# Kernel tuning notes

Measured on AMD Instinct MI355X. Metric: run time of the kernel, lower is better.

The kernel has to match this reference:

```python
import jax, jax.numpy as jnp
import numpy as np

N_NODES = 100000
N_EDGES = 800000
D_IN = 100
D_HID = 100
N_CLS = 16


def setup_inputs() -> dict:
    key = jax.random.key(0)
    ks = jax.random.split(key, 7)
    x = jax.random.normal(ks[0], (N_NODES, D_IN), dtype=jnp.float32)
    edge_index = jax.random.randint(ks[1], (2, N_EDGES), 0, N_NODES, dtype=jnp.int64)
    s = 1.0 / np.sqrt(D_IN)
    Wl = jax.random.normal(ks[2], (D_HID, D_IN), dtype=jnp.float32) * s
    bl = jax.random.normal(ks[3], (D_HID,), dtype=jnp.float32) * s
    Wr = jax.random.normal(ks[4], (D_HID, D_IN), dtype=jnp.float32) * s
    sc = 1.0 / np.sqrt(D_HID)
    Wc = jax.random.normal(ks[5], (N_CLS, D_HID), dtype=jnp.float32) * sc
    bc = jax.random.normal(ks[6], (N_CLS,), dtype=jnp.float32) * sc
    return {"x": x, "edge_index": edge_index, "Wl": Wl, "bl": bl,
            "Wr": Wr, "Wc": Wc, "bc": bc}


def reference(x, edge_index, Wl, bl, Wr, Wc, bc):
    # SAGEConv (mean aggregation): out_i = Wl @ mean_{j in N(i)} x_j + bl + Wr @ x_i
    src, dst = edge_index[0], edge_index[1]
    n = x.shape[0]
    agg = jax.ops.segment_sum(x[src], dst, num_segments=n)          # [N, D_IN]
    deg = jax.ops.segment_sum(jnp.ones((src.shape[0],), x.dtype), dst, num_segments=n)
    mean = agg / jnp.maximum(deg, 1.0)[:, None]
    h = mean @ Wl.T + bl + x @ Wr.T                                  # [N, D_HID]
    h = jax.nn.relu(h)
    out = h @ Wc.T + bc                                              # [N, N_CLS]
    return out
```

## Files before the change

### kernel.cpp

```cpp
#include <hip/hip_runtime.h>
#include <hip/hip_bf16.h>
#include <hip/hip_fp16.h>

#define N_NODES 100000
#define N_EDGES 800000
#define D_IN 100
#define D_HID 100
#define N_CLS 16

#define TN 64
#define SK 232
#define AK 200
#define SCHUNK 1024
#define SNBLK 98

typedef _Float16 f16x8 __attribute__((ext_vector_type(8)));
typedef _Float16 f16x4 __attribute__((ext_vector_type(4)));
typedef float f32x4 __attribute__((ext_vector_type(4)));

#define RANK_SLOT(e) (((e) >> 7) * AK + ((e) & 127))

__global__ __launch_bounds__(256) void hist_k(const int* __restrict__ ei,
                                              int* __restrict__ cnt,
                                              unsigned short* __restrict__ rank16)
{
    const int e = blockIdx.x * 256 + threadIdx.x;
    if (e < N_EDGES) {
        const int dst = ei[N_EDGES + e];
        const int r = atomicAdd(&cnt[dst], 1);
        rank16[RANK_SLOT(e)] = (unsigned short)r;
    }
}

__global__ __launch_bounds__(256) void scan_a(const int* __restrict__ cnt,
                                              int* __restrict__ bsum)
{
    __shared__ int red[256];
    const int t = threadIdx.x;
    const int base = blockIdx.x * SCHUNK + t * 4;
    int s = 0;
    if (base + 3 < N_NODES) {
        const int4 v = *reinterpret_cast<const int4*>(cnt + base);
        s = v.x + v.y + v.z + v.w;
    } else {
        for (int i = 0; i < 4; ++i)
            if (base + i < N_NODES) s += cnt[base + i];
    }
    red[t] = s;
    __syncthreads();
    for (int d = 128; d > 0; d >>= 1) {
        if (t < d) red[t] += red[t + d];
        __syncthreads();
    }
    if (t == 0) bsum[blockIdx.x] = red[0];
}

__global__ __launch_bounds__(256) void scan_c(const int* __restrict__ cnt,
                                              const int* __restrict__ bsum,
                                              int* __restrict__ wofs)
{
    __shared__ int red[256];
    __shared__ int sb[128];
    const int t = threadIdx.x;
    if (t < 128) sb[t] = (t < SNBLK) ? bsum[t] : 0;
    __syncthreads();
    for (int d = 1; d < 128; d <<= 1) {
        int a = 0;
        if (t < 128) { a = sb[t]; if (t >= d) a += sb[t - d]; }
        __syncthreads();
        if (t < 128) sb[t] = a;
        __syncthreads();
    }
    const int bofs = sb[blockIdx.x] - bsum[blockIdx.x];
    if (blockIdx.x == 0 && t == 0) wofs[N_NODES] = sb[SNBLK - 1];

    const int base = blockIdx.x * SCHUNK + t * 4;
    int c0 = 0, c1 = 0, c2 = 0, c3 = 0;
    if (base + 3 < N_NODES) {
        const int4 v = *reinterpret_cast<const int4*>(cnt + base);
        c0 = v.x; c1 = v.y; c2 = v.z; c3 = v.w;
    } else {
        if (base + 0 < N_NODES) c0 = cnt[base + 0];
        if (base + 1 < N_NODES) c1 = cnt[base + 1];
        if (base + 2 < N_NODES) c2 = cnt[base + 2];
        if (base + 3 < N_NODES) c3 = cnt[base + 3];
    }
    const int s = c0 + c1 + c2 + c3;
    red[t] = s;
    __syncthreads();
    for (int d = 1; d < 256; d <<= 1) {
        const int a = red[t];
        const int add = (t >= d) ? red[t - d] : 0;
        __syncthreads();
        red[t] = a + add;
        __syncthreads();
    }
    int prefix = bofs + red[t] - s;
    const int c[4] = {c0, c1, c2, c3};
    for (int i = 0; i < 4; ++i) {
        const int idx = base + i;
        if (idx < N_NODES) {
            wofs[idx] = prefix;
            prefix += c[i];
        }
    }
}

__global__ __launch_bounds__(256) void fill_csr(const int* __restrict__ ei,
                                                const int* __restrict__ wofs,
                                                const unsigned short* __restrict__ rank16,
                                                int* __restrict__ esrc)
{
    const int e = blockIdx.x * 256 + threadIdx.x;
    if (e >= N_EDGES) return;
    const int src = ei[e];
    const int dst = ei[N_EDGES + e];
    const int pos = wofs[dst] + (int)rank16[RANK_SLOT(e)];
    esrc[pos] = src;
}

__global__ __launch_bounds__(256) void cvt_w16(const float* __restrict__ Wl,
                                               const float* __restrict__ Wr,
                                               _Float16* __restrict__ w16)
{
    const int idx = blockIdx.x * 256 + threadIdx.x;
    if (idx >= 128 * 58) return;
    const int o = idx / 58, s = idx - o * 58;
    const int k0 = s * 4;
    float4 v = make_float4(0.f, 0.f, 0.f, 0.f);
    if (o < 100) {
        if (s < 25)       v = *reinterpret_cast<const float4*>(Wl + o * 100 + k0);
        else if (s < 50)  v = *reinterpret_cast<const float4*>(Wr + o * 100 + (k0 - 100));
    }
    f16x4 h = { (_Float16)v.x, (_Float16)v.y, (_Float16)v.z, (_Float16)v.w };
    *reinterpret_cast<f16x4*>(w16 + o * SK + k0) = h;
}

__global__ __launch_bounds__(256) void cvt_x16(const float* __restrict__ x,
                                               _Float16* __restrict__ amx)
{
    const int idx = blockIdx.x * 256 + threadIdx.x;
    if (idx >= N_NODES * 25) return;
    const int n = idx / 25, s = idx - n * 25;
    const float4 v = *reinterpret_cast<const float4*>(x + (long)n * D_IN + s * 4);
    f16x4 h = { (_Float16)v.x, (_Float16)v.y, (_Float16)v.z, (_Float16)v.w };
    *reinterpret_cast<f16x4*>(amx + (long)n * AK + 100 + s * 4) = h;
}

__global__ __launch_bounds__(256) void gather_mean(
    const int* __restrict__ wofs, const int* __restrict__ esrc,
    _Float16* __restrict__ amx)
{
    const int node = blockIdx.x * 8 + (threadIdx.x >> 5);
    if (node >= N_NODES) return;
    const int l = threadIdx.x & 31;
    const int r0 = wofs[node];
    const int r1 = wofs[node + 1];
    const int deg = r1 - r0;

    float4 acc = make_float4(0.f, 0.f, 0.f, 0.f);
    for (int base = 0; base < deg; base += 32) {
        int s = 0;
        if (base + l < deg) s = esrc[r0 + base + l];
        const int rem = deg - base;
        const int m = rem < 32 ? rem : 32;
        for (int j = 0; j < m; ++j) {
            const int src = __shfl(s, j, 32);
            if (l < 25) {
                const f16x4 v = *reinterpret_cast<const f16x4*>(
                    amx + (long)src * AK + 100 + l * 4);
                acc.x += (float)v[0]; acc.y += (float)v[1];
                acc.z += (float)v[2]; acc.w += (float)v[3];
            }
        }
    }
    if (l < 25) {
        const float inv = 1.0f / fmaxf((float)deg, 1.0f);
        f16x4 h = { (_Float16)(acc.x * inv), (_Float16)(acc.y * inv),
                    (_Float16)(acc.z * inv), (_Float16)(acc.w * inv) };
        *reinterpret_cast<f16x4*>(amx + (long)node * AK + l * 4) = h;
    }
}

__global__ __launch_bounds__(512, 1) void sage_node(
    const _Float16* __restrict__ amx, const _Float16* __restrict__ w16,
    const float* __restrict__ bl, const float* __restrict__ Wc,
    const float* __restrict__ bc, float* __restrict__ out)
{
    __shared__ __align__(16) _Float16 wS[128 * SK];
    __shared__ __align__(16) _Float16 aS[TN * SK];
    __shared__ float wcS[16 * 100];
    __shared__ float blS[128];
    __shared__ float bcS[16];

    const int tid = threadIdx.x;
    const int wid = tid >> 6;
    const int lane = tid & 63;
    const int node0 = blockIdx.x * TN;

    for (int c = tid; c < 128 * 29; c += 512) {
        const f16x8 v = *reinterpret_cast<const f16x8*>(w16 + c * 8);
        *reinterpret_cast<f16x8*>(wS + c * 8) = v;
    }
    {
        const f16x8 z = { (_Float16)0.f, (_Float16)0.f, (_Float16)0.f, (_Float16)0.f,
                          (_Float16)0.f, (_Float16)0.f, (_Float16)0.f, (_Float16)0.f };
        const _Float16* ga = amx + (size_t)node0 * AK;
        for (int c = tid; c < 64 * 29; c += 512) {
            const int row = c / 29, j = c - row * 29;
            f16x8 v = z;
            if (j < 25) v = *reinterpret_cast<const f16x8*>(ga + row * AK + j * 8);
            *reinterpret_cast<f16x8*>(aS + row * SK + j * 8) = v;
        }
    }
    for (int i = tid; i < 1600; i += 512) wcS[i] = Wc[i];
    if (tid < 128) blS[tid] = (tid < 100) ? bl[tid] : 0.0f;
    if (tid < 16)  bcS[tid] = bc[tid];
    __syncthreads();

    const int wr = wid >> 2;
    const int wq = wid & 3;
    const int lrow = lane & 15;
    const int lk = (lane >> 4) * 8;

    f32x4 acc00 = {0.f, 0.f, 0.f, 0.f}, acc01 = acc00, acc10 = acc00, acc11 = acc00;
    const _Float16* aB = aS + (wr * 32 + lrow) * SK + lk;
    const _Float16* bB = wS + (wq * 32 + lrow) * SK + lk;

    #pragma unroll
    for (int ks = 0; ks < 7; ++ks) {
        const f16x8 a0 = *reinterpret_cast<const f16x8*>(aB + ks * 32);
        const f16x8 a1 = *reinterpret_cast<const f16x8*>(aB + 16 * SK + ks * 32);
        const f16x8 b0 = *reinterpret_cast<const f16x8*>(bB + ks * 32);
        const f16x8 b1 = *reinterpret_cast<const f16x8*>(bB + 16 * SK + ks * 32);
        acc00 = __builtin_amdgcn_mfma_f32_16x16x32_f16(a0, b0, acc00, 0, 0, 0);
        acc01 = __builtin_amdgcn_mfma_f32_16x16x32_f16(a0, b1, acc01, 0, 0, 0);
        acc10 = __builtin_amdgcn_mfma_f32_16x16x32_f16(a1, b0, acc10, 0, 0, 0);
        acc11 = __builtin_amdgcn_mfma_f32_16x16x32_f16(a1, b1, acc11, 0, 0, 0);
    }
    __syncthreads();

    float* hS = reinterpret_cast<float*>(wS);
    const int crow = (lane >> 4) * 4;
    const int ccol = lane & 15;
    #pragma unroll
    for (int mi = 0; mi < 2; ++mi) {
        #pragma unroll
        for (int ni = 0; ni < 2; ++ni) {
            const f32x4 a = (mi == 0) ? (ni == 0 ? acc00 : acc01)
                                      : (ni == 0 ? acc10 : acc11);
            const int o = wq * 32 + ni * 16 + ccol;
            #pragma unroll
            for (int r = 0; r < 4; ++r) {
                const int nl = wr * 32 + mi * 16 + crow + r;
                if (o < 104)
                    hS[nl * 104 + o] = fmaxf(a[r] + blS[o], 0.0f);
            }
        }
    }
    __syncthreads();

    {
        const int nl = tid >> 3;
        const int q = tid & 7;
        float o0 = bcS[2 * q], o1 = bcS[2 * q + 1];
        const float* hP = hS + nl * 104;
        const float* w0 = wcS + (2 * q) * 100;
        const float* w1 = wcS + (2 * q + 1) * 100;
        for (int o = 0; o < 100; o += 4) {
            const float4 h4 = *reinterpret_cast<const float4*>(hP + o);
            const float4 a = *reinterpret_cast<const float4*>(w0 + o);
            const float4 b = *reinterpret_cast<const float4*>(w1 + o);
            o0 += h4.x * a.x + h4.y * a.y + h4.z * a.z + h4.w * a.w;
            o1 += h4.x * b.x + h4.y * b.y + h4.z * b.z + h4.w * b.w;
        }
        const int node = node0 + nl;
        if (node < N_NODES)
            *reinterpret_cast<float2*>(out + (long)node * N_CLS + 2 * q) =
                make_float2(o0, o1);
    }
}

extern "C" void kernel_launch(void* const* d_in, const int* in_sizes, int n_in,
                              void* d_out, int out_size, void* d_ws, size_t ws_size,
                              hipStream_t stream) {
    const float* x  = (const float*)d_in[0];
    const int*   ei = (const int*)d_in[1];
    const float* Wl = (const float*)d_in[2];
    const float* bl = (const float*)d_in[3];
    const float* Wr = (const float*)d_in[4];
    const float* Wc = (const float*)d_in[5];
    const float* bc = (const float*)d_in[6];
    float* out = (float*)d_out;

    int* cnt    = (int*)d_ws;
    int* wofs   = cnt + N_NODES;
    int* esrc   = wofs + N_NODES + 4;
    int* bsum   = esrc + N_EDGES;
    _Float16* w16 = (_Float16*)(bsum + 128);
    _Float16* amx = w16 + 128 * SK;
    unsigned short* rank16 = (unsigned short*)amx;

    hipMemsetAsync(cnt, 0, N_NODES * sizeof(int), stream);

    hist_k<<<(N_EDGES + 255) / 256, 256, 0, stream>>>(ei, cnt, rank16);
    scan_a<<<SNBLK, 256, 0, stream>>>(cnt, bsum);
    scan_c<<<SNBLK, 256, 0, stream>>>(cnt, bsum, wofs);
    fill_csr<<<(N_EDGES + 255) / 256, 256, 0, stream>>>(ei, wofs, rank16, esrc);
    cvt_w16<<<(128 * 58 + 255) / 256, 256, 0, stream>>>(Wl, Wr, w16);
    cvt_x16<<<(N_NODES * 25 + 255) / 256, 256, 0, stream>>>(x, amx);
    gather_mean<<<(N_NODES + 7) / 8, 256, 0, stream>>>(wofs, esrc, amx);

    sage_node<<<(N_NODES + TN - 1) / TN, 512, 0, stream>>>(
        amx, w16, bl, Wc, bc, out);
}
```

Measured before the change: 240.8 us.

## Merge prep kernels, double node tile, and use MFMA for classifier layer

Fuses the weight conversion into the scan-A kernel and the x conversion into the CSR fill kernel, cutting two launches and letting independent work run concurrently. The rank scratch slot mapping changes so it occupies only the mean columns of amx, avoiding a clash with the x columns that are now written in the same launch. The node kernel tile grows to 128 nodes so each wave does more MFMAs per weight load, and the hidden activations are stored as fp16 so the 16-class output layer runs on MFMA instead of scalar FMAs. This adds fp16 rounding of hidden activations and classifier weights, and uses more LDS per block.

```diff
diff --git a/kernel.cpp b/kernel.cpp
--- a/kernel.cpp
+++ b/kernel.cpp
@@ -8,17 +8,19 @@
 #define D_HID 100
 #define N_CLS 16
 
-#define TN 64
+#define TN 128
 #define SK 232
 #define AK 200
+#define HSTR 136
 #define SCHUNK 1024
 #define SNBLK 98
+#define FBLK 3125
 
 typedef _Float16 f16x8 __attribute__((ext_vector_type(8)));
 typedef _Float16 f16x4 __attribute__((ext_vector_type(4)));
 typedef float f32x4 __attribute__((ext_vector_type(4)));
 
-#define RANK_SLOT(e) (((e) >> 7) * AK + ((e) & 127))
+#define RANK_SLOT(e) (((e) / 100) * AK + ((e) % 100))
 
 __global__ __launch_bounds__(256) void hist_k(const int* __restrict__ ei,
                                               int* __restrict__ cnt,
@@ -32,27 +34,43 @@
     }
 }
 
-__global__ __launch_bounds__(256) void scan_a(const int* __restrict__ cnt,
-                                              int* __restrict__ bsum)
-{
-    __shared__ int red[256];
+__global__ __launch_bounds__(256) void scanA_cvtW(
+    const int* __restrict__ cnt, int* __restrict__ bsum,
+    const float* __restrict__ Wl, const float* __restrict__ Wr,
+    _Float16* __restrict__ w16)
+{
     const int t = threadIdx.x;
-    const int base = blockIdx.x * SCHUNK + t * 4;
-    int s = 0;
-    if (base + 3 < N_NODES) {
-        const int4 v = *reinterpret_cast<const int4*>(cnt + base);
-        s = v.x + v.y + v.z + v.w;
+    if (blockIdx.x < SNBLK) {
+        __shared__ int red[256];
+        const int base = blockIdx.x * SCHUNK + t * 4;
+        int s = 0;
+        if (base + 3 < N_NODES) {
+            const int4 v = *reinterpret_cast<const int4*>(cnt + base);
+            s = v.x + v.y + v.z + v.w;
+        } else {
+            for (int i = 0; i < 4; ++i)
+                if (base + i < N_NODES) s += cnt[base + i];
+        }
+        red[t] = s;
+        __syncthreads();
+        for (int d = 128; d > 0; d >>= 1) {
+            if (t < d) red[t] += red[t + d];
+            __syncthreads();
+        }
+        if (t == 0) bsum[blockIdx.x] = red[0];
     } else {
-        for (int i = 0; i < 4; ++i)
-            if (base + i < N_NODES) s += cnt[base + i];
-    }
-    red[t] = s;
-    __syncthreads();
-    for (int d = 128; d > 0; d >>= 1) {
-        if (t < d) red[t] += red[t + d];
-        __syncthreads();
-    }
-    if (t == 0) bsum[blockIdx.x] = red[0];
+        const int idx = (blockIdx.x - SNBLK) * 256 + t;
+        if (idx >= 128 * 58) return;
+        const int o = idx / 58, s = idx - o * 58;
+        const int k0 = s * 4;
+        float4 v = make_float4(0.f, 0.f, 0.f, 0.f);
+        if (o < 100) {
+            if (s < 25)       v = *reinterpret_cast<const float4*>(Wl + o * 100 + k0);
+            else if (s < 50)  v = *reinterpret_cast<const float4*>(Wr + o * 100 + (k0 - 100));
+        }
+        f16x4 h = { (_Float16)v.x, (_Float16)v.y, (_Float16)v.z, (_Float16)v.w };
+        *reinterpret_cast<f16x4*>(w16 + o * SK + k0) = h;
+    }
 }
 
 __global__ __launch_bounds__(256) void scan_c(const int* __restrict__ cnt,
@@ -106,45 +124,27 @@
     }
 }
 
-__global__ __launch_bounds__(256) void fill_csr(const int* __restrict__ ei,
-                                                const int* __restrict__ wofs,
-                                                const unsigned short* __restrict__ rank16,
-                                                int* __restrict__ esrc)
-{
-    const int e = blockIdx.x * 256 + threadIdx.x;
-    if (e >= N_EDGES) return;
-    const int src = ei[e];
-    const int dst = ei[N_EDGES + e];
-    const int pos = wofs[dst] + (int)rank16[RANK_SLOT(e)];
-    esrc[pos] = src;
-}
-
-__global__ __launch_bounds__(256) void cvt_w16(const float* __restrict__ Wl,
-                                               const float* __restrict__ Wr,
-                                               _Float16* __restrict__ w16)
-{
-    const int idx = blockIdx.x * 256 + threadIdx.x;
-    if (idx >= 128 * 58) return;
-    const int o = idx / 58, s = idx - o * 58;
-    const int k0 = s * 4;
-    float4 v = make_float4(0.f, 0.f, 0.f, 0.f);
-    if (o < 100) {
-        if (s < 25)       v = *reinterpret_cast<const float4*>(Wl + o * 100 + k0);
-        else if (s < 50)  v = *reinterpret_cast<const float4*>(Wr + o * 100 + (k0 - 100));
-    }
-    f16x4 h = { (_Float16)v.x, (_Float16)v.y, (_Float16)v.z, (_Float16)v.w };
-    *reinterpret_cast<f16x4*>(w16 + o * SK + k0) = h;
-}
-
-__global__ __launch_bounds__(256) void cvt_x16(const float* __restrict__ x,
-                                               _Float16* __restrict__ amx)
-{
-    const int idx = blockIdx.x * 256 + threadIdx.x;
-    if (idx >= N_NODES * 25) return;
-    const int n = idx / 25, s = idx - n * 25;
-    const float4 v = *reinterpret_cast<const float4*>(x + (long)n * D_IN + s * 4);
-    f16x4 h = { (_Float16)v.x, (_Float16)v.y, (_Float16)v.z, (_Float16)v.w };
-    *reinterpret_cast<f16x4*>(amx + (long)n * AK + 100 + s * 4) = h;
+__global__ __launch_bounds__(256) void fill_cvtX(
+    const int* __restrict__ ei, const int* __restrict__ wofs,
+    const unsigned short* __restrict__ rank16, int* __restrict__ esrc,
+    const float* __restrict__ x, _Float16* __restrict__ amx)
+{
+    const int t = threadIdx.x;
+    if (blockIdx.x < FBLK) {
+        const int e = blockIdx.x * 256 + t;
+        if (e >= N_EDGES) return;
+        const int src = ei[e];
+        const int dst = ei[N_EDGES + e];
+        const int pos = wofs[dst] + (int)rank16[RANK_SLOT(e)];
+        esrc[pos] = src;
+    } else {
+        const int idx = (blockIdx.x - FBLK) * 256 + t;
+        if (idx >= N_NODES * 25) return;
+        const int n = idx / 25, s = idx - n * 25;
+        const float4 v = *reinterpret_cast<const float4*>(x + (long)n * D_IN + s * 4);
+        f16x4 h = { (_Float16)v.x, (_Float16)v.y, (_Float16)v.z, (_Float16)v.w };
+        *reinterpret_cast<f16x4*>(amx + (long)n * AK + 100 + s * 4) = h;
+    }
 }
 
 __global__ __launch_bounds__(256) void gather_mean(
@@ -189,7 +189,7 @@
 {
     __shared__ __align__(16) _Float16 wS[128 * SK];
     __shared__ __align__(16) _Float16 aS[TN * SK];
-    __shared__ float wcS[16 * 100];
+    __shared__ __align__(16) _Float16 wc16[16 * HSTR];
     __shared__ float blS[128];
     __shared__ float bcS[16];
 
@@ -205,15 +205,19 @@
     {
         const f16x8 z = { (_Float16)0.f, (_Float16)0.f, (_Float16)0.f, (_Float16)0.f,
                           (_Float16)0.f, (_Float16)0.f, (_Float16)0.f, (_Float16)0.f };
-        const _Float16* ga = amx + (size_t)node0 * AK;
-        for (int c = tid; c < 64 * 29; c += 512) {
+        for (int c = tid; c < TN * 29; c += 512) {
             const int row = c / 29, j = c - row * 29;
             f16x8 v = z;
-            if (j < 25) v = *reinterpret_cast<const f16x8*>(ga + row * AK + j * 8);
+            if (j < 25 && node0 + row < N_NODES)
+                v = *reinterpret_cast<const f16x8*>(
+                    amx + (long)(node0 + row) * AK + j * 8);
             *reinterpret_cast<f16x8*>(aS + row * SK + j * 8) = v;
         }
     }
-    for (int i = tid; i < 1600; i += 512) wcS[i] = Wc[i];
+    for (int i = tid; i < 16 * HSTR; i += 512) {
+        const int cls = i / HSTR, k = i - cls * HSTR;
+        wc16[i] = (k < 100) ? (_Float16)Wc[cls * 100 + k] : (_Float16)0.f;
+    }
     if (tid < 128) blS[tid] = (tid < 100) ? bl[tid] : 0.0f;
     if (tid < 16)  bcS[tid] = bc[tid];
     __syncthreads();
@@ -223,61 +227,62 @@
     const int lrow = lane & 15;
     const int lk = (lane >> 4) * 8;
 
-    f32x4 acc00 = {0.f, 0.f, 0.f, 0.f}, acc01 = acc00, acc10 = acc00, acc11 = acc00;
-    const _Float16* aB = aS + (wr * 32 + lrow) * SK + lk;
+    f32x4 acc[4][2];
+    #pragma unroll
+    for (int mi = 0; mi < 4; ++mi)
+        #pragma unroll
+        for (int ni = 0; ni < 2; ++ni) acc[mi][ni] = (f32x4){0.f, 0.f, 0.f, 0.f};
+
+    const _Float16* aB = aS + (wr * 64 + lrow) * SK + lk;
     const _Float16* bB = wS + (wq * 32 + lrow) * SK + lk;
 
     #pragma unroll
     for (int ks = 0; ks < 7; ++ks) {
-        const f16x8 a0 = *reinterpret_cast<const f16x8*>(aB + ks * 32);
-        const f16x8 a1 = *reinterpret_cast<const f16x8*>(aB + 16 * SK + ks * 32);
         const f16x8 b0 = *reinterpret_cast<const f16x8*>(bB + ks * 32);
         const f16x8 b1 = *reinterpret_cast<const f16x8*>(bB + 16 * SK + ks * 32);
-        acc00 = __builtin_amdgcn_mfma_f32_16x16x32_f16(a0, b0, acc00, 0, 0, 0);
-        acc01 = __builtin_amdgcn_mfma_f32_16x16x32_f16(a0, b1, acc01, 0, 0, 0);
-        acc10 = __builtin_amdgcn_mfma_f32_16x16x32_f16(a1, b0, acc10, 0, 0, 0);
-        acc11 = __builtin_amdgcn_mfma_f32_16x16x32_f16(a1, b1, acc11, 0, 0, 0);
-    }
-    __syncthreads();
-
-    float* hS = reinterpret_cast<float*>(wS);
+        #pragma unroll
+        for (int mi = 0; mi < 4; ++mi) {
+            const f16x8 a = *reinterpret_cast<const f16x8*>(aB + mi * 16 * SK + ks * 32);
+            acc[mi][0] = __builtin_amdgcn_mfma_f32_16x16x32_f16(a, b0, acc[mi][0], 0, 0, 0);
+            acc[mi][1] = __builtin_amdgcn_mfma_f32_16x16x32_f16(a, b1, acc[mi][1], 0, 0, 0);
+        }
+    }
+    __syncthreads();
+
+    _Float16* hS = wS;
     const int crow = (lane >> 4) * 4;
     const int ccol = lane & 15;
     #pragma unroll
-    for (int mi = 0; mi < 2; ++mi) {
+    for (int mi = 0; mi < 4; ++mi) {
         #pragma unroll
         for (int ni = 0; ni < 2; ++ni) {
-            const f32x4 a = (mi == 0) ? (ni == 0 ? acc00 : acc01)
-                                      : (ni == 0 ? acc10 : acc11);
             const int o = wq * 32 + ni * 16 + ccol;
             #pragma unroll
             for (int r = 0; r < 4; ++r) {
-                const int nl = wr * 32 + mi * 16 + crow + r;
-                if (o < 104)
-                    hS[nl * 104 + o] = fmaxf(a[r] + blS[o], 0.0f);
+                const int rowl = wr * 64 + mi * 16 + crow + r;
+                hS[rowl * HSTR + o] = (_Float16)fmaxf(acc[mi][ni][r] + blS[o], 0.0f);
             }
         }
     }
     __syncthreads();
 
     {
-        const int nl = tid >> 3;
-        const int q = tid & 7;
-        float o0 = bcS[2 * q], o1 = bcS[2 * q + 1];
-        const float* hP = hS + nl * 104;
-        const float* w0 = wcS + (2 * q) * 100;
-        const float* w1 = wcS + (2 * q + 1) * 100;
-        for (int o = 0; o < 100; o += 4) {
-            const float4 h4 = *reinterpret_cast<const float4*>(hP + o);
-            const float4 a = *reinterpret_cast<const float4*>(w0 + o);
-            const float4 b = *reinterpret_cast<const float4*>(w1 + o);
-            o0 += h4.x * a.x + h4.y * a.y + h4.z * a.z + h4.w * a.w;
-            o1 += h4.x * b.x + h4.y * b.y + h4.z * b.z + h4.w * b.w;
-        }
-        const int node = node0 + nl;
-        if (node < N_NODES)
-            *reinterpret_cast<float2*>(out + (long)node * N_CLS + 2 * q) =
-                make_float2(o0, o1);
+        const _Float16* aR = hS + (wid * 16 + lrow) * HSTR + lk;
+        const _Float16* bR = wc16 + lrow * HSTR + lk;
+        f32x4 c4 = {0.f, 0.f, 0.f, 0.f};
+        #pragma unroll
+        for (int ks = 0; ks < 4; ++ks) {
+            const f16x8 a = *reinterpret_cast<const f16x8*>(aR + ks * 32);
+            const f16x8 b = *reinterpret_cast<const f16x8*>(bR + ks * 32);
+            c4 = __builtin_amdgcn_mfma_f32_16x16x32_f16(a, b, c4, 0, 0, 0);
+        }
+        const float bcv = bcS[lane & 15];
+        #pragma unroll
+        for (int r = 0; r < 4; ++r) {
+            const int node = node0 + wid * 16 + (lane >> 4) * 4 + r;
+            if (node < N_NODES)
+                out[(long)node * N_CLS + (lane & 15)] = c4[r] + bcv;
+        }
     }
 }
 
@@ -304,11 +309,10 @@
     hipMemsetAsync(cnt, 0, N_NODES * sizeof(int), stream);
 
     hist_k<<<(N_EDGES + 255) / 256, 256, 0, stream>>>(ei, cnt, rank16);
-    scan_a<<<SNBLK, 256, 0, stream>>>(cnt, bsum);
+    scanA_cvtW<<<SNBLK + 29, 256, 0, stream>>>(cnt, bsum, Wl, Wr, w16);
     scan_c<<<SNBLK, 256, 0, stream>>>(cnt, bsum, wofs);
-    fill_csr<<<(N_EDGES + 255) / 256, 256, 0, stream>>>(ei, wofs, rank16, esrc);
-    cvt_w16<<<(128 * 58 + 255) / 256, 256, 0, stream>>>(Wl, Wr, w16);
-    cvt_x16<<<(N_NODES * 25 + 255) / 256, 256, 0, stream>>>(x, amx);
+    fill_cvtX<<<FBLK + (N_NODES * 25 + 255) / 256, 256, 0, stream>>>(
+        ei, wofs, rank16, esrc, x, amx);
     gather_mean<<<(N_NODES + 7) / 8, 256, 0, stream>>>(wofs, esrc, amx);
 
     sage_node<<<(N_NODES + TN - 1) / TN, 512, 0, stream>>>(
```

New measurement: 225.6 us. -6.3%, faster.
